# Optimization experiments

Measured on AMD Instinct MI355X. Metric: run time of the kernel, lower is better.

Reference implementation:

```python
import jax, jax.numpy as jnp
import numpy as np
import math

THETA = 1.0


def _qdense(xa, xb, wa, wb, ba, bb):
    # QComplexDense: j_squared = -cos(2*theta)
    j2 = -math.cos(2.0 * THETA)
    out_a = xa @ wa.T + j2 * (xb @ wb.T) + ba
    out_b = xa @ wb.T + xb @ wa.T + bb
    return out_a, out_b


def setup_inputs() -> dict:
    key = jax.random.key(0)
    B, S, D = 4, 2048, 1024
    ks = jax.random.split(key, 16)
    limit = math.sqrt(6.0 / (D + D))  # xavier uniform for square [D,D]

    def w(k):
        return jax.random.uniform(k, (D, D), jnp.float32, -limit, limit)

    inp = {
        'xa': jax.random.normal(ks[0], (B, S, D), jnp.float32),
        'xb': jax.random.normal(ks[1], (B, S, D), jnp.float32),
    }
    i = 2
    for n in ('q', 'k', 'v', 'o'):
        inp[n + '_wa'] = w(ks[i]); inp[n + '_wb'] = w(ks[i + 1])
        inp[n + '_ba'] = jnp.zeros((D,), jnp.float32)
        inp[n + '_bb'] = jnp.zeros((D,), jnp.float32)
        i += 2
    return inp


def reference(xa, xb,
              q_wa, q_wb, q_ba, q_bb,
              k_wa, k_wb, k_ba, k_bb,
              v_wa, v_wb, v_ba, v_bb,
              o_wa, o_wb, o_ba, o_bb):
    D = xa.shape[-1]
    # NOTE: qc_matmul in the original uses cos(2 * ones(1)) == cos(2.0),
    # a constant independent of theta.
    c2 = math.cos(2.0)

    Qa, Qb = _qdense(xa, xb, q_wa, q_wb, q_ba, q_bb)
    Ka, Kb = _qdense(xa, xb, k_wa, k_wb, k_ba, k_bb)
    Va, Vb = _qdense(xa, xb, v_wa, v_wb, v_ba, v_bb)

    # complex-style QK^T: scores_a = Qa Ka^T - cos(2) Qb Kb^T ; scores_b = Qa Kb^T + Qb Ka^T
    sa = jnp.einsum('bsd,btd->bst', Qa, Ka) - c2 * jnp.einsum('bsd,btd->bst', Qb, Kb)
    sb = jnp.einsum('bsd,btd->bst', Qa, Kb) + jnp.einsum('bsd,btd->bst', Qb, Ka)
    scores_real = jnp.sqrt(sa * sa + sb * sb)  # magnitude
    attn = jax.nn.softmax(scores_real / math.sqrt(D), axis=-1)  # [B,S,S]

    out_a = jnp.einsum('bst,btd->bsd', attn, Va)
    out_b = jnp.einsum('bst,btd->bsd', attn, Vb)
    return _qdense(out_a, out_b, o_wa, o_wb, o_ba, o_bb)
```

## Files before the change

### kernel.cpp

```cpp
#include <hip/hip_runtime.h>
#include <math.h>

typedef __bf16 bf16_t;
typedef __attribute__((ext_vector_type(16))) float f32x16;
typedef __attribute__((ext_vector_type(8))) __bf16 v8bf;
typedef __attribute__((ext_vector_type(4))) __bf16 v4bf;

#define GLLDS(g, l)                                                           \
  __builtin_amdgcn_global_load_lds(                                           \
      (const __attribute__((address_space(1))) void*)(g),                     \
      (__attribute__((address_space(3))) void*)(l), 16, 0, 0)
#define OPQ(p) asm volatile("" : "+v"(p))

__global__ void sentinel_kernel(float* o, float v) { o[0] = v; }

__global__ __launch_bounds__(256) void pack_x_kernel(
    const float* __restrict__ xa, const float* __restrict__ xb,
    bf16_t* __restrict__ xcat, int n4)
{
  int i = blockIdx.x * 256 + threadIdx.x;
  if (i >= n4) return;
  float4 a = reinterpret_cast<const float4*>(xa)[i];
  float4 b = reinterpret_cast<const float4*>(xb)[i];
  long e = (long)i * 4;
  long m = e >> 10;
  int  d = (int)(e & 1023);
  v4bf av = { (bf16_t)a.x, (bf16_t)a.y, (bf16_t)a.z, (bf16_t)a.w };
  v4bf bv = { (bf16_t)b.x, (bf16_t)b.y, (bf16_t)b.z, (bf16_t)b.w };
  *reinterpret_cast<v4bf*>(xcat + m * 2048 + d)        = av;
  *reinterpret_cast<v4bf*>(xcat + m * 2048 + 1024 + d) = bv;
}

__global__ __launch_bounds__(256) void pack_w_kernel(
    const float* __restrict__ wa, const float* __restrict__ wb,
    bf16_t* __restrict__ outA, bf16_t* __restrict__ outB, float j2)
{
  int i = blockIdx.x * 256 + threadIdx.x;
  float4 a = reinterpret_cast<const float4*>(wa)[i];
  float4 b = reinterpret_cast<const float4*>(wb)[i];
  long e = (long)i * 4;
  long n = e >> 10;
  int  k = (int)(e & 1023);
  v4bf av = { (bf16_t)a.x, (bf16_t)a.y, (bf16_t)a.z, (bf16_t)a.w };
  v4bf bv = { (bf16_t)b.x, (bf16_t)b.y, (bf16_t)b.z, (bf16_t)b.w };
  v4bf jb = { (bf16_t)(j2*b.x), (bf16_t)(j2*b.y), (bf16_t)(j2*b.z), (bf16_t)(j2*b.w) };
  *reinterpret_cast<v4bf*>(outA + n * 2048 + k)        = av;
  *reinterpret_cast<v4bf*>(outA + n * 2048 + 1024 + k) = jb;
  *reinterpret_cast<v4bf*>(outB + n * 2048 + k)        = bv;
  *reinterpret_cast<v4bf*>(outB + n * 2048 + 1024 + k) = av;
}

template<int EPI>
__global__ __launch_bounds__(512) void gemm256_kernel(
    const bf16_t* __restrict__ A, const bf16_t* __restrict__ B,
    int K, long lda, long ldb, long bsA, long bsB,
    void* __restrict__ o0p, void* __restrict__ o1p, void* __restrict__ o2p,
    const float* __restrict__ bb0, const float* __restrict__ bb1,
    const float* __restrict__ bb2, const float* __restrict__ bb3,
    const float* __restrict__ bb4, const float* __restrict__ bb5,
    float scl)
{
  __shared__ __align__(16) bf16_t lds[65536];
  const int tid  = threadIdx.x;
  const int wid  = tid >> 6;
  const int lane = tid & 63;
  const int wm = wid >> 2;
  const int wn = wid & 3;

  const long row0 = (long)blockIdx.y * 256;
  const long col0 = (long)blockIdx.x * 256;
  const int z = blockIdx.z;
  const bf16_t* Ab = A + (long)z * bsA + row0 * lda;
  const bf16_t* Bb = B + (long)z * bsB + col0 * ldb;

  const int rhat = tid >> 2;
  const int scol = ((tid & 3) * 8) ^ (((rhat >> 1) & 3) << 3);
  const int dbase = wid * 512;

  const bf16_t* sA0 = Ab + (long)rhat * lda + scol;
  const bf16_t* sA1 = Ab + (long)(rhat + 128) * lda + scol;
  const bf16_t* sB0 = Bb + (long)rhat * ldb + scol;
  const bf16_t* sB1 = Bb + (long)(rhat + 128) * ldb + scol;

  const int r32 = lane & 31;
  const int kg2 = lane >> 5;
  const int swz = ((r32 >> 1) & 3) << 3;
  const int kq0 = (kg2 * 8) ^ swz;
  const bf16_t* pA[2] = { lds + (wm * 128 + r32) * 32 + kq0,
                          lds + (wm * 128 + r32) * 32 + (kq0 ^ 16) };
  const bf16_t* pB[2] = { lds + 8192 + (wn * 64 + r32) * 32 + kq0,
                          lds + 8192 + (wn * 64 + r32) * 32 + (kq0 ^ 16) };

  f32x16 acc[4][2];
#pragma unroll
  for (int i = 0; i < 4; ++i)
#pragma unroll
    for (int j = 0; j < 2; ++j)
#pragma unroll
      for (int e = 0; e < 16; ++e) acc[i][j][e] = 0.f;

  const int T = K >> 5;

  GLLDS(sA0, lds + dbase);
  GLLDS(sA1, lds + 4096 + dbase);
  GLLDS(sB0, lds + 8192 + dbase);
  GLLDS(sB1, lds + 12288 + dbase);
  sA0 += 32; sA1 += 32; sB0 += 32; sB1 += 32;
  OPQ(sA0); OPQ(sA1); OPQ(sB0); OPQ(sB1);
  GLLDS(sA0, lds + 16384 + dbase);
  GLLDS(sA1, lds + 16384 + 4096 + dbase);
  GLLDS(sB0, lds + 16384 + 8192 + dbase);
  GLLDS(sB1, lds + 16384 + 12288 + dbase);
  sA0 += 32; sA1 += 32; sB0 += 32; sB1 += 32;
  OPQ(sA0); OPQ(sA1); OPQ(sB0); OPQ(sB1);
  asm volatile("s_waitcnt vmcnt(4)" ::: "memory");
  __builtin_amdgcn_sched_barrier(0);
  __builtin_amdgcn_s_barrier();

#define TILE_BODY(U, PF)                                                       \
  {                                                                            \
    const int so_ = ((U) < 2 ? 0 : 32768) + ((U) & 1) * 16384;                 \
    v8bf af_[2][2], bf_[2][2], ag_[2][2];                                      \
    _Pragma("unroll") for (int f = 0; f < 2; ++f)                              \
      _Pragma("unroll") for (int s = 0; s < 2; ++s)                            \
        bf_[f][s] = *reinterpret_cast<const v8bf*>(pB[s] + so_ + f * 1024);    \
    _Pragma("unroll") for (int f = 0; f < 2; ++f)                              \
      _Pragma("unroll") for (int s = 0; s < 2; ++s)                            \
        af_[f][s] = *reinterpret_cast<const v8bf*>(pA[s] + so_ + f * 1024);    \
    _Pragma("unroll") for (int f = 0; f < 2; ++f)                              \
      _Pragma("unroll") for (int s = 0; s < 2; ++s)                            \
        ag_[f][s] = *reinterpret_cast<const v8bf*>(pA[s] + so_ + (2 + f) * 1024); \
    if (PF) {                                                                  \
      GLLDS(sA0, lds + (((U) + 2) & 3) * 16384 + dbase);                       \
      GLLDS(sA1, lds + (((U) + 2) & 3) * 16384 + 4096 + dbase);                \
      GLLDS(sB0, lds + (((U) + 2) & 3) * 16384 + 8192 + dbase);                \
      GLLDS(sB1, lds + (((U) + 2) & 3) * 16384 + 12288 + dbase);               \
    }                                                                          \
    __builtin_amdgcn_s_setprio(1);                                             \
    _Pragma("unroll") for (int s = 0; s < 2; ++s)                              \
      _Pragma("unroll") for (int f = 0; f < 2; ++f)                            \
        _Pragma("unroll") for (int g = 0; g < 2; ++g)                          \
          acc[f][g] = __builtin_amdgcn_mfma_f32_32x32x16_bf16(af_[f][s], bf_[g][s], acc[f][g], 0, 0, 0); \
    _Pragma("unroll") for (int s = 0; s < 2; ++s)                              \
      _Pragma("unroll") for (int f = 0; f < 2; ++f)                            \
        _Pragma("unroll") for (int g = 0; g < 2; ++g)                          \
          acc[2 + f][g] = __builtin_amdgcn_mfma_f32_32x32x16_bf16(ag_[f][s], bf_[g][s], acc[2 + f][g], 0, 0, 0); \
    __builtin_amdgcn_s_setprio(0);                                             \
    if (PF) {                                                                  \
      sA0 += 32; sA1 += 32; sB0 += 32; sB1 += 32;                              \
      OPQ(sA0); OPQ(sA1); OPQ(sB0); OPQ(sB1);                                  \
    }                                                                          \
    if (PF) { asm volatile("s_waitcnt vmcnt(4)" ::: "memory"); }               \
    else    { asm volatile("s_waitcnt vmcnt(0)" ::: "memory"); }               \
    __builtin_amdgcn_sched_barrier(0);                                         \
    __builtin_amdgcn_s_barrier();                                              \
  }

  for (int tb = 0; tb < T - 4; tb += 4) {
    TILE_BODY(0, 1)
    TILE_BODY(1, 1)
    TILE_BODY(2, 1)
    TILE_BODY(3, 1)
  }
  TILE_BODY(0, 1)
  TILE_BODY(1, 1)
  TILE_BODY(2, 0)
  TILE_BODY(3, 0)
#undef TILE_BODY

  const int hi = lane >> 5;
#pragma unroll
  for (int fm = 0; fm < 4; ++fm) {
#pragma unroll
    for (int fn = 0; fn < 2; ++fn) {
      const f32x16 v = acc[fm][fn];
      const long rowb = row0 + wm * 128 + fm * 32 + 4 * hi;
      const long col  = col0 + wn * 64 + fn * 32 + r32;
      if constexpr (EPI == 0) {
        const int  seg = (int)(col >> 10);
        const long c   = col & 1023;
        bf16_t* Q  = (bf16_t*)o0p;
        bf16_t* Kc = (bf16_t*)o1p;
        bf16_t* Vc = (bf16_t*)o2p;
        switch (seg) {
          case 0: { const float bv = bb0[c];
#pragma unroll
            for (int r = 0; r < 16; ++r) {
              const long row = rowb + (r & 3) + 8 * (r >> 2);
              Q[row * 2048 + c] = (bf16_t)((v[r] + bv) * 0.03125f);
            } } break;
          case 1: { const float bv = bb1[c];
#pragma unroll
            for (int r = 0; r < 16; ++r) {
              const long row = rowb + (r & 3) + 8 * (r >> 2);
              Q[row * 2048 + 1024 + c] = (bf16_t)((v[r] + bv) * 0.03125f);
            } } break;
          case 2: { const float bv = bb2[c];
#pragma unroll
            for (int r = 0; r < 16; ++r) {
              const long row = rowb + (r & 3) + 8 * (r >> 2);
              const long kbase = (row >> 11) * 8388608 + (row & 2047) * 2048;
              const float w = v[r] + bv;
              Kc[kbase + c]                  = (bf16_t)w;
              Kc[kbase + 4194304 + 1024 + c] = (bf16_t)w;
            } } break;
          case 3: { const float bv = bb3[c];
#pragma unroll
            for (int r = 0; r < 16; ++r) {
              const long row = rowb + (r & 3) + 8 * (r >> 2);
              const long kbase = (row >> 11) * 8388608 + (row & 2047) * 2048;
              const float w = v[r] + bv;
              Kc[kbase + 4194304 + c] = (bf16_t)w;
              Kc[kbase + 1024 + c]    = (bf16_t)(scl * w);
            } } break;
          case 4: { const float bv = bb4[c];
#pragma unroll
            for (int r = 0; r < 16; ++r) {
              const long row = rowb + (r & 3) + 8 * (r >> 2);
              Vc[row * 2048 + c] = (bf16_t)(v[r] + bv);
            } } break;
          default: { const float bv = bb5[c];
#pragma unroll
            for (int r = 0; r < 16; ++r) {
              const long row = rowb + (r & 3) + 8 * (r >> 2);
              Vc[row * 2048 + 1024 + c] = (bf16_t)(v[r] + bv);
            } } break;
        }
      } else if constexpr (EPI == 1) {
        const int  seg = (int)(col >> 11);
        const long c   = col & 2047;
        bf16_t* dst = seg ? (bf16_t*)o1p : (bf16_t*)o0p;
#pragma unroll
        for (int r = 0; r < 16; ++r) {
          const long row = rowb + (r & 3) + 8 * (r >> 2);
          dst[(long)z * 4194304 + row * 2048 + c] = (bf16_t)v[r];
        }
      } else if constexpr (EPI == 2) {
#pragma unroll
        for (int r = 0; r < 16; ++r) {
          const long row = rowb + (r & 3) + 8 * (r >> 2);
          ((bf16_t*)o0p)[(long)z * 4194304 + row * 2048 + col] = (bf16_t)v[r];
        }
      } else {
        const int  seg = (int)(col >> 10);
        const long c   = col & 1023;
        float* dst = seg ? (float*)o1p : (float*)o0p;
        const float bv = seg ? bb1[c] : bb0[c];
#pragma unroll
        for (int r = 0; r < 16; ++r) {
          const long row = rowb + (r & 3) + 8 * (r >> 2);
          dst[row * 1024 + c] = v[r] + bv;
        }
      }
    }
  }
}

__global__ __launch_bounds__(256) void transpose_v_kernel(
    const bf16_t* __restrict__ src, bf16_t* __restrict__ dst)
{
  __shared__ bf16_t t[64][65];
  const int tid = threadIdx.x;
  const int off = blockIdx.z * 1024;
  const long c0 = (long)blockIdx.x * 64;
  const long g0 = (long)blockIdx.y * 64;
#pragma unroll
  for (int it = 0; it < 16; ++it) {
    int idx = it * 256 + tid;
    int r = idx >> 6, c = idx & 63;
    t[r][c] = src[(g0 + r) * 2048 + off + c0 + c];
  }
  __syncthreads();
  const long b  = g0 >> 11;
  const long t0 = g0 & 2047;
#pragma unroll
  for (int it = 0; it < 16; ++it) {
    int idx = it * 256 + tid;
    int nr = idx >> 6, tc = idx & 63;
    dst[b * 4194304 + (off + c0 + nr) * 2048 + t0 + tc] = t[tc][nr];
  }
}

__global__ __launch_bounds__(256) void softmax_mag_kernel(
    const bf16_t* __restrict__ sa, const bf16_t* __restrict__ sb,
    bf16_t* __restrict__ attn)
{
  const int tid = threadIdx.x;
  const long base = (long)blockIdx.x * 2048;
  v4bf a0 = *reinterpret_cast<const v4bf*>(sa + base + tid * 4);
  v4bf a1 = *reinterpret_cast<const v4bf*>(sa + base + 1024 + tid * 4);
  v4bf b0 = *reinterpret_cast<const v4bf*>(sb + base + tid * 4);
  v4bf b1 = *reinterpret_cast<const v4bf*>(sb + base + 1024 + tid * 4);
  float r[8];
#pragma unroll
  for (int k = 0; k < 4; ++k) {
    float x = (float)a0[k], y = (float)b0[k];
    r[k] = sqrtf(x * x + y * y);
  }
#pragma unroll
  for (int k = 0; k < 4; ++k) {
    float x = (float)a1[k], y = (float)b1[k];
    r[4 + k] = sqrtf(x * x + y * y);
  }
  float m = r[0];
#pragma unroll
  for (int k = 1; k < 8; ++k) m = fmaxf(m, r[k]);
#pragma unroll
  for (int off = 32; off > 0; off >>= 1) m = fmaxf(m, __shfl_xor(m, off));
  __shared__ float red[8];
  if ((tid & 63) == 0) red[tid >> 6] = m;
  __syncthreads();
  m = fmaxf(fmaxf(red[0], red[1]), fmaxf(red[2], red[3]));
  float p[8], s = 0.f;
#pragma unroll
  for (int k = 0; k < 8; ++k) { p[k] = __expf(r[k] - m); s += p[k]; }
#pragma unroll
  for (int off = 32; off > 0; off >>= 1) s += __shfl_xor(s, off);
  if ((tid & 63) == 0) red[4 + (tid >> 6)] = s;
  __syncthreads();
  const float inv = 1.f / (red[4] + red[5] + red[6] + red[7]);
  v4bf o0 = { (bf16_t)(p[0]*inv), (bf16_t)(p[1]*inv), (bf16_t)(p[2]*inv), (bf16_t)(p[3]*inv) };
  v4bf o1 = { (bf16_t)(p[4]*inv), (bf16_t)(p[5]*inv), (bf16_t)(p[6]*inv), (bf16_t)(p[7]*inv) };
  *reinterpret_cast<v4bf*>(attn + base + tid * 4)        = o0;
  *reinterpret_cast<v4bf*>(attn + base + 1024 + tid * 4) = o1;
}

extern "C" void kernel_launch(void* const* d_in, const int* in_sizes, int n_in,
                              void* d_out, int out_size, void* d_ws, size_t ws_size,
                              hipStream_t stream)
{
  (void)in_sizes; (void)n_in; (void)out_size;
  const float* xa = (const float*)d_in[0];
  const float* xb = (const float*)d_in[1];
  const float *w_a[4], *w_b[4], *b_a[4], *b_b[4];
  for (int p = 0; p < 4; ++p) {
    w_a[p] = (const float*)d_in[2 + p*4 + 0];
    w_b[p] = (const float*)d_in[2 + p*4 + 1];
    b_a[p] = (const float*)d_in[2 + p*4 + 2];
    b_b[p] = (const float*)d_in[2 + p*4 + 3];
  }
  float* out = (float*)d_out;
  const float neg_c2 = (float)(-cos(2.0));

  const size_t WFULL = 33554432ull;
  const size_t WQKV  = 25165824ull;
  int NB = 0; bool fullW = true;
  if      (ws_size >= WFULL + 6ull * 4ull * 8388608ull) NB = 4;
  else if (ws_size >= WFULL + 6ull * 2ull * 8388608ull) NB = 2;
  else if (ws_size >= WFULL + 6ull * 1ull * 8388608ull) NB = 1;
  else if (ws_size >= WQKV  + 6ull * 1ull * 8388608ull) { NB = 1; fullW = false; }
  else { sentinel_kernel<<<1, 1, 0, stream>>>(out, (float)ws_size); return; }

  char* ws = (char*)d_ws;
  const size_t wbytes = fullW ? WFULL : WQKV;
  const size_t RB = (size_t)NB * 8388608ull;
  bf16_t* Wqkv = (bf16_t*)ws;
  bf16_t* Wo   = fullW ? (bf16_t*)(ws + WQKV) : Wqkv;
  bf16_t* R0 = (bf16_t*)(ws + wbytes);
  bf16_t* R1 = (bf16_t*)(ws + wbytes + 1*RB);
  bf16_t* Kc = (bf16_t*)(ws + wbytes + 2*RB);
  bf16_t* R4 = (bf16_t*)(ws + wbytes + 4*RB);
  bf16_t* R5 = (bf16_t*)(ws + wbytes + 5*RB);

  const int  Mc = NB * 2048;
  const dim3 blk(256);
  const dim3 blk512(512);
  const dim3 gqkv(24, Mc / 256, 1);
  const dim3 gsc(16, 8, NB);
  const dim3 gpv(8, 8, NB);
  const dim3 go(8, Mc / 256, 1);
  const dim3 gtr(16, Mc / 64, 2);

  if (fullW) {
    for (int p = 0; p < 3; ++p)
      pack_w_kernel<<<1024, blk, 0, stream>>>(w_a[p], w_b[p],
          Wqkv + (size_t)(2*p)   * 2097152ull,
          Wqkv + (size_t)(2*p+1) * 2097152ull, neg_c2);
    pack_w_kernel<<<1024, blk, 0, stream>>>(w_a[3], w_b[3],
        Wo, Wo + 2097152ull, neg_c2);
  }

  for (int c = 0; c < 4 / NB; ++c) {
    const size_t xoff = (size_t)c * NB * 2097152ull;
    pack_x_kernel<<<Mc, blk, 0, stream>>>(xa + xoff, xb + xoff, R0, Mc * 256);

    if (!fullW)
      for (int p = 0; p < 3; ++p)
        pack_w_kernel<<<1024, blk, 0, stream>>>(w_a[p], w_b[p],
            Wqkv + (size_t)(2*p)   * 2097152ull,
            Wqkv + (size_t)(2*p+1) * 2097152ull, neg_c2);

    gemm256_kernel<0><<<gqkv, blk512, 0, stream>>>(R0, Wqkv, 2048, 2048, 2048, 0, 0,
        R1, Kc, R4, b_a[0], b_b[0], b_a[1], b_b[1], b_a[2], b_b[2], neg_c2);

    transpose_v_kernel<<<gtr, blk, 0, stream>>>(R4, R5);

    gemm256_kernel<1><<<gsc, blk512, 0, stream>>>(R1, Kc, 2048, 2048, 2048, 4194304, 8388608,
        R0, R4, nullptr, nullptr, nullptr, nullptr, nullptr, nullptr, nullptr, 0.f);

    softmax_mag_kernel<<<Mc, blk, 0, stream>>>(R0, R4, R0);

    gemm256_kernel<2><<<gpv, blk512, 0, stream>>>(R0, R5, 2048, 2048, 2048, 4194304, 4194304,
        R1, nullptr, nullptr, nullptr, nullptr, nullptr, nullptr, nullptr, nullptr, 0.f);

    if (!fullW)
      pack_w_kernel<<<1024, blk, 0, stream>>>(w_a[3], w_b[3], Wo, Wo + 2097152ull, neg_c2);
    gemm256_kernel<3><<<go, blk512, 0, stream>>>(R1, Wo, 2048, 2048, 2048, 0, 0,
        out + xoff, out + 8388608ull + xoff, nullptr,
        b_a[3], b_b[3], nullptr, nullptr, nullptr, nullptr, 0.f);
  }
}
```

Measured before the change: 574.3 us.

## Process two K-tiles per barrier in the bf16 MFMA GEMM main loop

Restructures the GEMM main loop so that each barrier step covers two 32-wide K tiles instead of one. Both tiles' global-to-LDS prefetches are issued together, and the second tile's LDS fragment reads are interleaved between MFMA groups of the first. This halves the number of workgroup barriers and vmcnt waits. In exchange, every step now waits with vmcnt(0), which drains all outstanding loads and shortens the effective prefetch lead. The loop trip count is also hardcoded for K=2048, so it would break silently for any other K.

```diff
diff --git a/kernel.cpp b/kernel.cpp
--- a/kernel.cpp
+++ b/kernel.cpp
@@ -100,6 +100,7 @@
       for (int e = 0; e < 16; ++e) acc[i][j][e] = 0.f;
 
   const int T = K >> 5;
+  (void)T;
 
   GLLDS(sA0, lds + dbase);
   GLLDS(sA1, lds + 4096 + dbase);
@@ -113,60 +114,85 @@
   GLLDS(sB1, lds + 16384 + 12288 + dbase);
   sA0 += 32; sA1 += 32; sB0 += 32; sB1 += 32;
   OPQ(sA0); OPQ(sA1); OPQ(sB0); OPQ(sB1);
-  asm volatile("s_waitcnt vmcnt(4)" ::: "memory");
+  asm volatile("s_waitcnt vmcnt(0)" ::: "memory");
   __builtin_amdgcn_sched_barrier(0);
   __builtin_amdgcn_s_barrier();
 
-#define TILE_BODY(U, PF)                                                       \
+#define PAIR_BODY(U0, U1, PF)                                                  \
   {                                                                            \
-    const int so_ = ((U) < 2 ? 0 : 32768) + ((U) & 1) * 16384;                 \
-    v8bf af_[2][2], bf_[2][2], ag_[2][2];                                      \
-    _Pragma("unroll") for (int f = 0; f < 2; ++f)                              \
-      _Pragma("unroll") for (int s = 0; s < 2; ++s)                            \
-        bf_[f][s] = *reinterpret_cast<const v8bf*>(pB[s] + so_ + f * 1024);    \
-    _Pragma("unroll") for (int f = 0; f < 2; ++f)                              \
-      _Pragma("unroll") for (int s = 0; s < 2; ++s)                            \
-        af_[f][s] = *reinterpret_cast<const v8bf*>(pA[s] + so_ + f * 1024);    \
-    _Pragma("unroll") for (int f = 0; f < 2; ++f)                              \
-      _Pragma("unroll") for (int s = 0; s < 2; ++s)                            \
-        ag_[f][s] = *reinterpret_cast<const v8bf*>(pA[s] + so_ + (2 + f) * 1024); \
+    const int so0_ = (U0) * 16384;                                             \
+    const int so1_ = (U1) * 16384;                                             \
+    v8bf a0_[2][2], b0_[2][2], g0_[2][2];                                      \
+    v8bf a1_[2][2], b1_[2][2], g1_[2][2];                                      \
+                                         \
+    _Pragma("unroll") for (int f = 0; f < 2; ++f)                              \
+      _Pragma("unroll") for (int s = 0; s < 2; ++s)                            \
+        b0_[f][s] = *reinterpret_cast<const v8bf*>(pB[s] + so0_ + f * 1024);   \
+    _Pragma("unroll") for (int f = 0; f < 2; ++f)                              \
+      _Pragma("unroll") for (int s = 0; s < 2; ++s)                            \
+        a0_[f][s] = *reinterpret_cast<const v8bf*>(pA[s] + so0_ + f * 1024);   \
+    _Pragma("unroll") for (int f = 0; f < 2; ++f)                              \
+      _Pragma("unroll") for (int s = 0; s < 2; ++s)                            \
+        g0_[f][s] = *reinterpret_cast<const v8bf*>(pA[s] + so0_ + (2 + f) * 1024); \
+       \
     if (PF) {                                                                  \
-      GLLDS(sA0, lds + (((U) + 2) & 3) * 16384 + dbase);                       \
-      GLLDS(sA1, lds + (((U) + 2) & 3) * 16384 + 4096 + dbase);                \
-      GLLDS(sB0, lds + (((U) + 2) & 3) * 16384 + 8192 + dbase);                \
-      GLLDS(sB1, lds + (((U) + 2) & 3) * 16384 + 12288 + dbase);               \
+      GLLDS(sA0, lds + (((U0) + 2) & 3) * 16384 + dbase);                      \
+      GLLDS(sA1, lds + (((U0) + 2) & 3) * 16384 + 4096 + dbase);               \
+      GLLDS(sB0, lds + (((U0) + 2) & 3) * 16384 + 8192 + dbase);               \
+      GLLDS(sB1, lds + (((U0) + 2) & 3) * 16384 + 12288 + dbase);              \
+      sA0 += 32; sA1 += 32; sB0 += 32; sB1 += 32;                              \
+      OPQ(sA0); OPQ(sA1); OPQ(sB0); OPQ(sB1);                                  \
+      GLLDS(sA0, lds + (((U1) + 2) & 3) * 16384 + dbase);                      \
+      GLLDS(sA1, lds + (((U1) + 2) & 3) * 16384 + 4096 + dbase);               \
+      GLLDS(sB0, lds + (((U1) + 2) & 3) * 16384 + 8192 + dbase);               \
+      GLLDS(sB1, lds + (((U1) + 2) & 3) * 16384 + 12288 + dbase);              \
+      sA0 += 32; sA1 += 32; sB0 += 32; sB1 += 32;                              \
+      OPQ(sA0); OPQ(sA1); OPQ(sB0); OPQ(sB1);                                  \
     }                                                                          \
+                               \
     __builtin_amdgcn_s_setprio(1);                                             \
     _Pragma("unroll") for (int s = 0; s < 2; ++s)                              \
       _Pragma("unroll") for (int f = 0; f < 2; ++f)                            \
         _Pragma("unroll") for (int g = 0; g < 2; ++g)                          \
-          acc[f][g] = __builtin_amdgcn_mfma_f32_32x32x16_bf16(af_[f][s], bf_[g][s], acc[f][g], 0, 0, 0); \
+          acc[f][g] = __builtin_amdgcn_mfma_f32_32x32x16_bf16(a0_[f][s], b0_[g][s], acc[f][g], 0, 0, 0); \
+    __builtin_amdgcn_s_setprio(0);                                             \
+      \
+    _Pragma("unroll") for (int f = 0; f < 2; ++f)                              \
+      _Pragma("unroll") for (int s = 0; s < 2; ++s)                            \
+        b1_[f][s] = *reinterpret_cast<const v8bf*>(pB[s] + so1_ + f * 1024);   \
+    _Pragma("unroll") for (int f = 0; f < 2; ++f)                              \
+      _Pragma("unroll") for (int s = 0; s < 2; ++s)                            \
+        a1_[f][s] = *reinterpret_cast<const v8bf*>(pA[s] + so1_ + f * 1024);   \
+    _Pragma("unroll") for (int f = 0; f < 2; ++f)                              \
+      _Pragma("unroll") for (int s = 0; s < 2; ++s)                            \
+        g1_[f][s] = *reinterpret_cast<const v8bf*>(pA[s] + so1_ + (2 + f) * 1024); \
+       \
+    __builtin_amdgcn_s_setprio(1);                                             \
     _Pragma("unroll") for (int s = 0; s < 2; ++s)                              \
       _Pragma("unroll") for (int f = 0; f < 2; ++f)                            \
         _Pragma("unroll") for (int g = 0; g < 2; ++g)                          \
-          acc[2 + f][g] = __builtin_amdgcn_mfma_f32_32x32x16_bf16(ag_[f][s], bf_[g][s], acc[2 + f][g], 0, 0, 0); \
+          acc[2 + f][g] = __builtin_amdgcn_mfma_f32_32x32x16_bf16(g0_[f][s], b0_[g][s], acc[2 + f][g], 0, 0, 0); \
+    _Pragma("unroll") for (int s = 0; s < 2; ++s)                              \
+      _Pragma("unroll") for (int f = 0; f < 2; ++f)                            \
+        _Pragma("unroll") for (int g = 0; g < 2; ++g)                          \
+          acc[f][g] = __builtin_amdgcn_mfma_f32_32x32x16_bf16(a1_[f][s], b1_[g][s], acc[f][g], 0, 0, 0); \
+    _Pragma("unroll") for (int s = 0; s < 2; ++s)                              \
+      _Pragma("unroll") for (int f = 0; f < 2; ++f)                            \
+        _Pragma("unroll") for (int g = 0; g < 2; ++g)                          \
+          acc[2 + f][g] = __builtin_amdgcn_mfma_f32_32x32x16_bf16(g1_[f][s], b1_[g][s], acc[2 + f][g], 0, 0, 0); \
     __builtin_amdgcn_s_setprio(0);                                             \
-    if (PF) {                                                                  \
-      sA0 += 32; sA1 += 32; sB0 += 32; sB1 += 32;                              \
-      OPQ(sA0); OPQ(sA1); OPQ(sB0); OPQ(sB1);                                  \
-    }                                                                          \
-    if (PF) { asm volatile("s_waitcnt vmcnt(4)" ::: "memory"); }               \
-    else    { asm volatile("s_waitcnt vmcnt(0)" ::: "memory"); }               \
+    asm volatile("s_waitcnt vmcnt(0)" ::: "memory");                           \
     __builtin_amdgcn_sched_barrier(0);                                         \
     __builtin_amdgcn_s_barrier();                                              \
   }
 
-  for (int tb = 0; tb < T - 4; tb += 4) {
-    TILE_BODY(0, 1)
-    TILE_BODY(1, 1)
-    TILE_BODY(2, 1)
-    TILE_BODY(3, 1)
-  }
-  TILE_BODY(0, 1)
-  TILE_BODY(1, 1)
-  TILE_BODY(2, 0)
-  TILE_BODY(3, 0)
-#undef TILE_BODY
+  for (int tb = 0; tb < 60; tb += 4) {
+    PAIR_BODY(0, 1, 1)
+    PAIR_BODY(2, 3, 1)
+  }
+  PAIR_BODY(0, 1, 1)
+  PAIR_BODY(2, 3, 0)
+#undef PAIR_BODY
 
   const int hi = lane >> 5;
 #pragma unroll
```

Result: no change. 576.4 us (+0.4%).

## Switch GEMM mainloop to BK=64 double-buffered tiles with XOR-8 swizzle

Applied to the files above, without the earlier changes.

The GEMM main loop goes from a 4-stage ring of 32-wide K tiles to a 2-stage double buffer of 64-wide K tiles, with each wave loading 8 rows of 64 columns and an 8-chunk XOR swizzle in LDS. Each iteration splits into two half-steps that interleave the A and B prefetches of the next tile with the MFMA work, and barriers now occur every 64 K. This halves barrier count and lengthens the load transactions, but it waits with vmcnt(0) every step, so prefetch depth drops and memory latency is less hidden.

```diff
diff --git a/kernel.cpp b/kernel.cpp
--- a/kernel.cpp
+++ b/kernel.cpp
@@ -73,23 +73,29 @@
   const bf16_t* Ab = A + (long)z * bsA + row0 * lda;
   const bf16_t* Bb = B + (long)z * bsB + col0 * ldb;
 
-  const int rhat = tid >> 2;
-  const int scol = ((tid & 3) * 8) ^ (((rhat >> 1) & 3) << 3);
+  const int srow = wid * 8 + (lane >> 3);
+  const int scol = ((lane & 7) ^ (lane >> 3)) * 8;
   const int dbase = wid * 512;
 
-  const bf16_t* sA0 = Ab + (long)rhat * lda + scol;
-  const bf16_t* sA1 = Ab + (long)(rhat + 128) * lda + scol;
-  const bf16_t* sB0 = Bb + (long)rhat * ldb + scol;
-  const bf16_t* sB1 = Bb + (long)(rhat + 128) * ldb + scol;
+  const bf16_t* sA0 = Ab + (long)srow * lda + scol;
+  const bf16_t* sA1 = Ab + (long)(srow + 64) * lda + scol;
+  const bf16_t* sA2 = Ab + (long)(srow + 128) * lda + scol;
+  const bf16_t* sA3 = Ab + (long)(srow + 192) * lda + scol;
+  const bf16_t* sB0 = Bb + (long)srow * ldb + scol;
+  const bf16_t* sB1 = Bb + (long)(srow + 64) * ldb + scol;
+  const bf16_t* sB2 = Bb + (long)(srow + 128) * ldb + scol;
+  const bf16_t* sB3 = Bb + (long)(srow + 192) * ldb + scol;
 
   const int r32 = lane & 31;
   const int kg2 = lane >> 5;
-  const int swz = ((r32 >> 1) & 3) << 3;
-  const int kq0 = (kg2 * 8) ^ swz;
-  const bf16_t* pA[2] = { lds + (wm * 128 + r32) * 32 + kq0,
-                          lds + (wm * 128 + r32) * 32 + (kq0 ^ 16) };
-  const bf16_t* pB[2] = { lds + 8192 + (wn * 64 + r32) * 32 + kq0,
-                          lds + 8192 + (wn * 64 + r32) * 32 + (kq0 ^ 16) };
+  const int r7 = r32 & 7;
+  const bf16_t *pAs[4], *pBs[4];
+#pragma unroll
+  for (int s = 0; s < 4; ++s) {
+    const int ch = (((kg2 + 2 * s) ^ r7) & 7) * 8;
+    pAs[s] = lds + (wm * 128 + r32) * 64 + ch;
+    pBs[s] = lds + 16384 + (wn * 64 + r32) * 64 + ch;
+  }
 
   f32x16 acc[4][2];
 #pragma unroll
@@ -99,73 +105,82 @@
 #pragma unroll
       for (int e = 0; e < 16; ++e) acc[i][j][e] = 0.f;
 
-  const int T = K >> 5;
+  const int T = K >> 6;
 
   GLLDS(sA0, lds + dbase);
   GLLDS(sA1, lds + 4096 + dbase);
-  GLLDS(sB0, lds + 8192 + dbase);
-  GLLDS(sB1, lds + 12288 + dbase);
-  sA0 += 32; sA1 += 32; sB0 += 32; sB1 += 32;
-  OPQ(sA0); OPQ(sA1); OPQ(sB0); OPQ(sB1);
-  GLLDS(sA0, lds + 16384 + dbase);
-  GLLDS(sA1, lds + 16384 + 4096 + dbase);
-  GLLDS(sB0, lds + 16384 + 8192 + dbase);
-  GLLDS(sB1, lds + 16384 + 12288 + dbase);
-  sA0 += 32; sA1 += 32; sB0 += 32; sB1 += 32;
-  OPQ(sA0); OPQ(sA1); OPQ(sB0); OPQ(sB1);
-  asm volatile("s_waitcnt vmcnt(4)" ::: "memory");
+  GLLDS(sA2, lds + 8192 + dbase);
+  GLLDS(sA3, lds + 12288 + dbase);
+  GLLDS(sB0, lds + 16384 + dbase);
+  GLLDS(sB1, lds + 16384 + 4096 + dbase);
+  GLLDS(sB2, lds + 16384 + 8192 + dbase);
+  GLLDS(sB3, lds + 16384 + 12288 + dbase);
+  sA0 += 64; sA1 += 64; sA2 += 64; sA3 += 64;
+  sB0 += 64; sB1 += 64; sB2 += 64; sB3 += 64;
+  OPQ(sA0); OPQ(sA1); OPQ(sA2); OPQ(sA3);
+  OPQ(sB0); OPQ(sB1); OPQ(sB2); OPQ(sB3);
+  asm volatile("s_waitcnt vmcnt(0)" ::: "memory");
   __builtin_amdgcn_sched_barrier(0);
   __builtin_amdgcn_s_barrier();
 
 #define TILE_BODY(U, PF)                                                       \
   {                                                                            \
-    const int so_ = ((U) < 2 ? 0 : 32768) + ((U) & 1) * 16384;                 \
-    v8bf af_[2][2], bf_[2][2], ag_[2][2];                                      \
-    _Pragma("unroll") for (int f = 0; f < 2; ++f)                              \
-      _Pragma("unroll") for (int s = 0; s < 2; ++s)                            \
-        bf_[f][s] = *reinterpret_cast<const v8bf*>(pB[s] + so_ + f * 1024);    \
-    _Pragma("unroll") for (int f = 0; f < 2; ++f)                              \
-      _Pragma("unroll") for (int s = 0; s < 2; ++s)                            \
-        af_[f][s] = *reinterpret_cast<const v8bf*>(pA[s] + so_ + f * 1024);    \
-    _Pragma("unroll") for (int f = 0; f < 2; ++f)                              \
-      _Pragma("unroll") for (int s = 0; s < 2; ++s)                            \
-        ag_[f][s] = *reinterpret_cast<const v8bf*>(pA[s] + so_ + (2 + f) * 1024); \
+    const int so_ = (U) * 32768;                                               \
+    const int ns_ = (1 - (U)) * 32768;                                         \
+    v8bf a_[4][2], b_[2][2];                                                   \
+                                             \
+    _Pragma("unroll") for (int g = 0; g < 2; ++g)                              \
+      _Pragma("unroll") for (int ss = 0; ss < 2; ++ss)                         \
+        b_[g][ss] = *reinterpret_cast<const v8bf*>(pBs[ss] + so_ + g * 2048);  \
+    _Pragma("unroll") for (int f = 0; f < 4; ++f)                              \
+      _Pragma("unroll") for (int ss = 0; ss < 2; ++ss)                         \
+        a_[f][ss] = *reinterpret_cast<const v8bf*>(pAs[ss] + so_ + f * 2048);  \
     if (PF) {                                                                  \
-      GLLDS(sA0, lds + (((U) + 2) & 3) * 16384 + dbase);                       \
-      GLLDS(sA1, lds + (((U) + 2) & 3) * 16384 + 4096 + dbase);                \
-      GLLDS(sB0, lds + (((U) + 2) & 3) * 16384 + 8192 + dbase);                \
-      GLLDS(sB1, lds + (((U) + 2) & 3) * 16384 + 12288 + dbase);               \
+      GLLDS(sA0, lds + ns_ + dbase);                                           \
+      GLLDS(sA1, lds + ns_ + 4096 + dbase);                                    \
+      GLLDS(sA2, lds + ns_ + 8192 + dbase);                                    \
+      GLLDS(sA3, lds + ns_ + 12288 + dbase);                                   \
     }                                                                          \
     __builtin_amdgcn_s_setprio(1);                                             \
-    _Pragma("unroll") for (int s = 0; s < 2; ++s)                              \
-      _Pragma("unroll") for (int f = 0; f < 2; ++f)                            \
+    _Pragma("unroll") for (int ss = 0; ss < 2; ++ss)                           \
+      _Pragma("unroll") for (int f = 0; f < 4; ++f)                            \
         _Pragma("unroll") for (int g = 0; g < 2; ++g)                          \
-          acc[f][g] = __builtin_amdgcn_mfma_f32_32x32x16_bf16(af_[f][s], bf_[g][s], acc[f][g], 0, 0, 0); \
-    _Pragma("unroll") for (int s = 0; s < 2; ++s)                              \
-      _Pragma("unroll") for (int f = 0; f < 2; ++f)                            \
+          acc[f][g] = __builtin_amdgcn_mfma_f32_32x32x16_bf16(a_[f][ss], b_[g][ss], acc[f][g], 0, 0, 0); \
+    __builtin_amdgcn_s_setprio(0);                                             \
+                                             \
+    _Pragma("unroll") for (int g = 0; g < 2; ++g)                              \
+      _Pragma("unroll") for (int ss = 0; ss < 2; ++ss)                         \
+        b_[g][ss] = *reinterpret_cast<const v8bf*>(pBs[2 + ss] + so_ + g * 2048); \
+    _Pragma("unroll") for (int f = 0; f < 4; ++f)                              \
+      _Pragma("unroll") for (int ss = 0; ss < 2; ++ss)                         \
+        a_[f][ss] = *reinterpret_cast<const v8bf*>(pAs[2 + ss] + so_ + f * 2048); \
+    if (PF) {                                                                  \
+      GLLDS(sB0, lds + ns_ + 16384 + dbase);                                   \
+      GLLDS(sB1, lds + ns_ + 16384 + 4096 + dbase);                            \
+      GLLDS(sB2, lds + ns_ + 16384 + 8192 + dbase);                            \
+      GLLDS(sB3, lds + ns_ + 16384 + 12288 + dbase);                           \
+      sA0 += 64; sA1 += 64; sA2 += 64; sA3 += 64;                              \
+      sB0 += 64; sB1 += 64; sB2 += 64; sB3 += 64;                              \
+      OPQ(sA0); OPQ(sA1); OPQ(sA2); OPQ(sA3);                                  \
+      OPQ(sB0); OPQ(sB1); OPQ(sB2); OPQ(sB3);                                  \
+    }                                                                          \
+    __builtin_amdgcn_s_setprio(1);                                             \
+    _Pragma("unroll") for (int ss = 0; ss < 2; ++ss)                           \
+      _Pragma("unroll") for (int f = 0; f < 4; ++f)                            \
         _Pragma("unroll") for (int g = 0; g < 2; ++g)                          \
-          acc[2 + f][g] = __builtin_amdgcn_mfma_f32_32x32x16_bf16(ag_[f][s], bf_[g][s], acc[2 + f][g], 0, 0, 0); \
+          acc[f][g] = __builtin_amdgcn_mfma_f32_32x32x16_bf16(a_[f][ss], b_[g][ss], acc[f][g], 0, 0, 0); \
     __builtin_amdgcn_s_setprio(0);                                             \
-    if (PF) {                                                                  \
-      sA0 += 32; sA1 += 32; sB0 += 32; sB1 += 32;                              \
-      OPQ(sA0); OPQ(sA1); OPQ(sB0); OPQ(sB1);                                  \
-    }                                                                          \
-    if (PF) { asm volatile("s_waitcnt vmcnt(4)" ::: "memory"); }               \
-    else    { asm volatile("s_waitcnt vmcnt(0)" ::: "memory"); }               \
+    asm volatile("s_waitcnt vmcnt(0)" ::: "memory");                           \
     __builtin_amdgcn_sched_barrier(0);                                         \
     __builtin_amdgcn_s_barrier();                                              \
   }
 
-  for (int tb = 0; tb < T - 4; tb += 4) {
+  for (int tb = 0; tb < T - 2; tb += 2) {
     TILE_BODY(0, 1)
     TILE_BODY(1, 1)
-    TILE_BODY(2, 1)
-    TILE_BODY(3, 1)
   }
   TILE_BODY(0, 1)
-  TILE_BODY(1, 1)
-  TILE_BODY(2, 0)
-  TILE_BODY(3, 0)
+  TILE_BODY(1, 0)
 #undef TILE_BODY
 
   const int hi = lane >> 5;
```

Result: faster. 559.6 us (-2.6%).
